# Kernel tuning notes

Measured on AMD Instinct MI355X. Metric: run time of the kernel, lower is better.

Reference implementation:

```python
import jax, jax.numpy as jnp
import numpy as np

D_MODEL = 256
D_STATE = 16
D_INNER = 512          # expand=2 * d_model
D_CONV = 4
DT_RANK = 16           # ceil(d_model/16)
B, L = 16, 2048


def setup_inputs() -> dict:
    key = jax.random.key(0)
    ks = jax.random.split(key, 10)
    s = 0.02
    inp = {
        "x": jax.random.normal(ks[0], (B, L, D_MODEL), dtype=jnp.float32),
        "ln_w": jnp.ones((D_MODEL,), jnp.float32),
        "ln_b": jnp.zeros((D_MODEL,), jnp.float32),
        "in_proj_w": jax.random.normal(ks[1], (2 * D_INNER, D_MODEL)) * s,
        "conv_w": jax.random.normal(ks[2], (D_INNER, 1, D_CONV)) * s,
        "conv_b": jnp.zeros((D_INNER,), jnp.float32),
        "x_proj_w": jax.random.normal(ks[3], (DT_RANK + 2 * D_STATE, D_INNER)) * s,
        "dt_proj_w": jax.random.normal(ks[4], (D_INNER, DT_RANK)) * s,
        "dt_proj_b": jax.random.uniform(ks[5], (D_INNER,), minval=-4.0, maxval=-2.0),
        "A_log": jnp.log(jnp.broadcast_to(jnp.arange(1, D_STATE + 1, dtype=jnp.float32), (D_INNER, D_STATE))).copy(),
        "D_param": jnp.ones((D_INNER,), jnp.float32),
        "out_proj_w": jax.random.normal(ks[6], (D_MODEL, D_INNER)) * s,
    }
    return inp


def _layernorm(x, w, b, eps=1e-5):
    mu = jnp.mean(x, axis=-1, keepdims=True)
    var = jnp.var(x, axis=-1, keepdims=True)
    return (x - mu) * jax.lax.rsqrt(var + eps) * w + b


def _mamba(xn, in_proj_w, conv_w, conv_b, x_proj_w, dt_proj_w, dt_proj_b, A_log, D_param, out_proj_w):
    # in_proj -> x, z   (B, L, d_inner) each
    xz = jnp.einsum('bld,ed->ble', xn, in_proj_w)
    x_in, z = jnp.split(xz, 2, axis=-1)

    # depthwise causal conv over L
    xc = jax.lax.conv_general_dilated(
        jnp.transpose(x_in, (0, 2, 1)), conv_w,
        window_strides=(1,), padding=[(D_CONV - 1, 0)],
        feature_group_count=D_INNER,
        dimension_numbers=('NCH', 'OIH', 'NCH')) + conv_b[None, :, None]
    xc = jax.nn.silu(jnp.transpose(xc, (0, 2, 1)))  # (B, L, d_inner)

    # input-dependent dt, B, C
    dbc = jnp.einsum('ble,fe->blf', xc, x_proj_w)  # (B, L, dt_rank + 2N)
    dt = jax.nn.softplus(jnp.einsum('blr,er->ble', dbc[..., :DT_RANK], dt_proj_w) + dt_proj_b)
    Bc = dbc[..., DT_RANK:DT_RANK + D_STATE]   # (B, L, N)
    Cc = dbc[..., DT_RANK + D_STATE:]          # (B, L, N)

    A = -jnp.exp(A_log)  # (d_inner, N)

    def step(h, inputs):
        dt_t, x_t, B_t, C_t = inputs  # (B,e), (B,e), (B,n), (B,n)
        dA = jnp.exp(dt_t[..., None] * A)                      # (B, e, n)
        h = dA * h + dt_t[..., None] * B_t[:, None, :] * x_t[..., None]
        y = jnp.sum(h * C_t[:, None, :], axis=-1)              # (B, e)
        return h, y

    h0 = jnp.zeros((xn.shape[0], D_INNER, D_STATE), xn.dtype)
    seq = (jnp.swapaxes(dt, 0, 1), jnp.swapaxes(xc, 0, 1),
           jnp.swapaxes(Bc, 0, 1), jnp.swapaxes(Cc, 0, 1))
    _, ys = jax.lax.scan(step, h0, seq)
    y = jnp.swapaxes(ys, 0, 1) + D_param * xc                  # (B, L, e)
    y = y * jax.nn.silu(z)
    return jnp.einsum('ble,de->bld', y, out_proj_w)


def reference(x, ln_w, ln_b, in_proj_w, conv_w, conv_b, x_proj_w, dt_proj_w, dt_proj_b, A_log, D_param, out_proj_w):
    xn = _layernorm(x, ln_w, ln_b)
    out = _mamba(xn, in_proj_w, conv_w, conv_b, x_proj_w, dt_proj_w, dt_proj_b, A_log, D_param, out_proj_w)
    return x + out  # dropout is identity in eval
```

## Files before the change

kernel.cpp:

```cpp
#include <hip/hip_runtime.h>
#include <cstdint>

#define DEVI __device__ __forceinline__

typedef __bf16 bf16;
typedef __bf16 bf16x8 __attribute__((ext_vector_type(8)));
typedef __bf16 bf16x4 __attribute__((ext_vector_type(4)));
typedef __bf16 bf16x2 __attribute__((ext_vector_type(2)));
typedef float floatx4 __attribute__((ext_vector_type(4)));
typedef float f32x2 __attribute__((ext_vector_type(2)));

constexpr int BATCH = 16, SEQ = 2048, DM = 256, DI = 512;
constexpr int M = BATCH * SEQ;
constexpr int NC = 64;
constexpr int CL = SEQ / NC;
static_assert(NC * CL == SEQ, "chunking");
constexpr float LOG2E = 1.4426950408889634f;

DEVI void gl2lds16(const void* g, void* l) {
  __builtin_amdgcn_global_load_lds(
      (const __attribute__((address_space(1))) unsigned int*)(uintptr_t)g,
      (__attribute__((address_space(3))) unsigned int*)(unsigned int)(uintptr_t)l,
      16, 0, 0);
}

DEVI float sigmoidf_(float x) { return 1.f / (1.f + __expf(-x)); }
DEVI float exp2_(float x) { return __builtin_amdgcn_exp2f(x); }

DEVI float bflo(unsigned u) { return __uint_as_float(u << 16); }
DEVI float bfhi(unsigned u) { return __uint_as_float(u & 0xFFFF0000u); }
DEVI f32x2 sp2(float v) { f32x2 r; r[0] = v; r[1] = v; return r; }

DEVI void powseq(f32x2 d, f32x2* P) {
  P[0] = d;
  P[1] = d * d;
  P[2] = P[1] * d;
  P[3] = P[1] * P[1];
  P[4] = P[3] * d;
  P[5] = P[3] * P[1];
  P[6] = P[3] * P[2];
  P[7] = P[3] * P[3];
  P[8] = P[7] * d;
  P[9] = P[7] * P[1];
  P[10] = P[7] * P[2];
  P[11] = P[7] * P[3];
  P[12] = P[7] * P[4];
  P[13] = P[7] * P[5];
  P[14] = P[7] * P[6];
  P[15] = P[7] * P[7];
}

__global__ __launch_bounds__(256) void prep_kernel(
    const float* __restrict__ w1, const float* __restrict__ wx,
    const float* __restrict__ wo, const float* __restrict__ alog,
    bf16* __restrict__ w1b, bf16* __restrict__ wxb, bf16* __restrict__ wob,
    float* __restrict__ An, int* __restrict__ flags) {
  constexpr int n1 = 1024 * 256, n2 = 48 * 512, n3 = 256 * 512;
  int i = blockIdx.x * 256 + threadIdx.x;
  if (i < n1) w1b[i] = (bf16)w1[i];
  else if (i < n1 + n2) wxb[i - n1] = (bf16)wx[i - n1];
  else if (i < n1 + n2 + n3) wob[i - n1 - n2] = (bf16)wo[i - n1 - n2];
  else if (i < n1 + n2 + n3 + DI) {
    const int e = i - (n1 + n2 + n3);
    const float a0 = -__expf(alog[e * 16]);
    bool ok = (a0 < 0.f);
#pragma unroll 1
    for (int s = 0; s < 16; s++) {
      const float a = -__expf(alog[e * 16 + s]);
      An[e * 16 + s] = a * LOG2E;
      ok = ok && (__builtin_fabsf(a / a0 - (float)(s + 1)) < 1e-3f);
    }
    flags[e] = ok ? 1 : 0;
  }
}

__global__ __launch_bounds__(256) void ln_kernel(
    const float* __restrict__ x, const float* __restrict__ w,
    const float* __restrict__ b, bf16* __restrict__ xn) {
  const int row = blockIdx.x * 4 + (threadIdx.x >> 6);
  const int lane = threadIdx.x & 63;
  const float4 v = ((const float4*)(x + (size_t)row * DM))[lane];
  float s = v.x + v.y + v.z + v.w;
  float s2 = v.x * v.x + v.y * v.y + v.z * v.z + v.w * v.w;
#pragma unroll
  for (int m = 1; m < 64; m <<= 1) { s += __shfl_xor(s, m); s2 += __shfl_xor(s2, m); }
  const float mu = s * (1.f / DM);
  const float var = s2 * (1.f / DM) - mu * mu;
  const float rs = rsqrtf(var + 1e-5f);
  const float4 wv = ((const float4*)w)[lane];
  const float4 bv = ((const float4*)b)[lane];
  bf16x4 o;
  o[0] = (bf16)((v.x - mu) * rs * wv.x + bv.x);
  o[1] = (bf16)((v.y - mu) * rs * wv.y + bv.y);
  o[2] = (bf16)((v.z - mu) * rs * wv.z + bv.z);
  o[3] = (bf16)((v.w - mu) * rs * wv.w + bv.w);
  *(bf16x4*)(xn + (size_t)row * DM + lane * 4) = o;
}

template <int N, int K, bool OUT_BF16, bool RESID>
__global__ __launch_bounds__(256) void gemm_nt(const bf16* __restrict__ A,
                                               const bf16* __restrict__ W,
                                               void* __restrict__ out,
                                               const float* __restrict__ resid) {
  constexpr int BK = 32;
  __shared__ __align__(16) bf16 lA[128 * BK];
  __shared__ __align__(16) bf16 lB[128 * BK];
  const int tid = threadIdx.x;
  const int wave = tid >> 6, lane = tid & 63;
  const int bm = blockIdx.x * 128, bn = blockIdx.y * 128;
  const int wm = (wave >> 1) * 64, wn = (wave & 1) * 64;
  const int q = lane >> 4, r = lane & 15;
  floatx4 acc[4][4] = {};
  const int c0 = wave * 64 + lane;
  const int row0 = c0 >> 2, kp = (c0 & 3) * 8;
  for (int k0 = 0; k0 < K; k0 += BK) {
    gl2lds16(A + (size_t)(bm + row0) * K + k0 + kp, lA + c0 * 8);
    gl2lds16(A + (size_t)(bm + row0 + 64) * K + k0 + kp, lA + (c0 + 256) * 8);
    gl2lds16(W + (size_t)(bn + row0) * K + k0 + kp, lB + c0 * 8);
    gl2lds16(W + (size_t)(bn + row0 + 64) * K + k0 + kp, lB + (c0 + 256) * 8);
    __syncthreads();
    bf16x8 af[4], bfr[4];
#pragma unroll
    for (int i = 0; i < 4; i++) af[i] = *(const bf16x8*)&lA[(wm + i * 16 + r) * BK + q * 8];
#pragma unroll
    for (int j = 0; j < 4; j++) bfr[j] = *(const bf16x8*)&lB[(wn + j * 16 + r) * BK + q * 8];
#pragma unroll
    for (int i = 0; i < 4; i++)
#pragma unroll
      for (int j = 0; j < 4; j++)
        acc[i][j] = __builtin_amdgcn_mfma_f32_16x16x32_bf16(af[i], bfr[j], acc[i][j], 0, 0, 0);
    __syncthreads();
  }
#pragma unroll
  for (int i = 0; i < 4; i++)
#pragma unroll
    for (int j = 0; j < 4; j++)
#pragma unroll
      for (int t = 0; t < 4; t++) {
        const int row = bm + wm + i * 16 + q * 4 + t;
        const int col = bn + wn + j * 16 + r;
        const size_t idx = (size_t)row * N + col;
        float v = acc[i][j][t];
        if constexpr (OUT_BF16) {
          ((bf16*)out)[idx] = (bf16)v;
        } else {
          if constexpr (RESID) v += resid[idx];
          ((float*)out)[idx] = v;
        }
      }
}

__global__ __launch_bounds__(256) void conv_silu(const bf16* __restrict__ xz,
                                                 const float* __restrict__ cw,
                                                 const float* __restrict__ cb,
                                                 bf16* __restrict__ xc) {
  const int tid = threadIdx.x;
  const int e2 = tid * 2;
  const int p0 = blockIdx.x * 8;
  const int b = blockIdx.y;
  const float4 w0 = ((const float4*)cw)[e2];
  const float4 w1 = ((const float4*)cw)[e2 + 1];
  const float2 bias = *(const float2*)(cb + e2);
  float xa[11], xb_[11];
#pragma unroll
  for (int j = 0; j < 11; j++) {
    const int pos = p0 - 3 + j;
    float fa = 0.f, fb = 0.f;
    if (pos >= 0) {
      const unsigned u = *(const unsigned*)(xz + ((size_t)b * SEQ + pos) * 1024 + e2);
      fa = __uint_as_float(u << 16);
      fb = __uint_as_float(u & 0xFFFF0000u);
    }
    xa[j] = fa; xb_[j] = fb;
  }
#pragma unroll
  for (int k = 0; k < 8; k++) {
    const float a0 = bias.x + xa[k] * w0.x + xa[k + 1] * w0.y + xa[k + 2] * w0.z + xa[k + 3] * w0.w;
    const float a1 = bias.y + xb_[k] * w1.x + xb_[k + 1] * w1.y + xb_[k + 2] * w1.z + xb_[k + 3] * w1.w;
    bf16x2 o;
    o[0] = (bf16)(a0 * sigmoidf_(a0));
    o[1] = (bf16)(a1 * sigmoidf_(a1));
    *(bf16x2*)(xc + ((size_t)b * SEQ + p0 + k) * DI + e2) = o;
  }
}

__global__ __launch_bounds__(256) void gemm_xproj(const bf16* __restrict__ A,
                                                  const bf16* __restrict__ W,
                                                  float* __restrict__ out) {
  constexpr int K = DI;
  __shared__ __align__(16) bf16 lW[48 * K];
  __shared__ __align__(16) bf16 lA[64 * 32];
  const int tid = threadIdx.x;
  const int wave = tid >> 6, lane = tid & 63;
  const int bm = blockIdx.x * 64;
  const int q = lane >> 4, r = lane & 15;
#pragma unroll
  for (int rd = 0; rd < 12; rd++) {
    const int c = rd * 256 + tid;
    gl2lds16((const char*)W + (size_t)c * 16, (char*)lW + (size_t)c * 16);
  }
  const int row0 = tid >> 2, kp = (tid & 3) * 8;
  const int wm = wave * 16;
  floatx4 acc[3] = {};
  for (int k0 = 0; k0 < K; k0 += 32) {
    gl2lds16(A + (size_t)(bm + row0) * K + k0 + kp, lA + tid * 8);
    __syncthreads();
    bf16x8 af = *(const bf16x8*)&lA[(wm + r) * 32 + q * 8];
#pragma unroll
    for (int j = 0; j < 3; j++) {
      const bf16x8 bfr = *(const bf16x8*)&lW[(j * 16 + r) * K + k0 + q * 8];
      acc[j] = __builtin_amdgcn_mfma_f32_16x16x32_bf16(af, bfr, acc[j], 0, 0, 0);
    }
    __syncthreads();
  }
#pragma unroll
  for (int j = 0; j < 3; j++)
#pragma unroll
    for (int t = 0; t < 4; t++)
      out[(size_t)(bm + wm + q * 4 + t) * 48 + j * 16 + r] = acc[j][t];
}

__global__ __launch_bounds__(256) void dtproj_kernel(const float* __restrict__ dbc,
                                                     const float* __restrict__ dtw,
                                                     const float* __restrict__ dtb,
                                                     bf16* __restrict__ dt) {
  __shared__ __align__(16) float sd[64 * 16];
  const int tid = threadIdx.x;
  const int p0 = blockIdx.x * 64;
  const int e = blockIdx.y * 256 + tid;
  {
    const int rowi = tid >> 2, coli = (tid & 3) * 4;
    *(float4*)&sd[rowi * 16 + coli] = *(const float4*)(dbc + (size_t)(p0 + rowi) * 48 + coli);
  }
  float w[16];
#pragma unroll
  for (int s = 0; s < 16; s += 4) {
    float4 t4 = *(const float4*)(dtw + (size_t)e * 16 + s);
    w[s] = t4.x; w[s + 1] = t4.y; w[s + 2] = t4.z; w[s + 3] = t4.w;
  }
  const float bias = dtb[e];
  __syncthreads();
  for (int p = 0; p < 64; p++) {
    float s = bias;
#pragma unroll
    for (int r2 = 0; r2 < 16; r2++) s += sd[p * 16 + r2] * w[r2];
    const float sp = (s > 15.f) ? s : __logf(1.f + __expf(s));
    dt[(size_t)(p0 + p) * DI + e] = (bf16)sp;
  }
}

__global__ __launch_bounds__(256) void scan_pass1(const bf16* __restrict__ dt,
                                                  const bf16* __restrict__ xc,
                                                  const float* __restrict__ dbc,
                                                  const float* __restrict__ An,
                                                  const int* __restrict__ flags,
                                                  float* __restrict__ U,
                                                  float* __restrict__ SD) {
  __shared__ __align__(16) float sbc[CL * 16];
  const int tid = threadIdx.x;
  const int e2 = tid * 2;
  const int ch = blockIdx.x, b = blockIdx.y;
  const size_t posBase = (size_t)b * SEQ + (size_t)ch * CL;
  if (tid < CL * 4) {
    const int il = tid >> 2, f = (tid & 3) * 4;
    gl2lds16(dbc + (posBase + il) * 48 + 16 + f, (char*)sbc + tid * 16);
  }
  const int2 fl = *(const int2*)(flags + e2);
  const int fast = fl.x & fl.y;
  f32x2 h[16];
#pragma unroll
  for (int s = 0; s < 16; s++) { h[s][0] = 0.f; h[s][1] = 0.f; }
  f32x2 sdt2; sdt2[0] = 0.f; sdt2[1] = 0.f;
  f32x2 A02; A02[0] = An[(size_t)e2 * 16]; A02[1] = An[(size_t)e2 * 16 + 16];
  float Aa[16], Ab[16];
  if (!fast) {
#pragma unroll
    for (int s = 0; s < 16; s += 4) {
      float4 a4 = *(const float4*)(An + (size_t)e2 * 16 + s);
      Aa[s] = a4.x; Aa[s + 1] = a4.y; Aa[s + 2] = a4.z; Aa[s + 3] = a4.w;
      float4 b4 = *(const float4*)(An + (size_t)e2 * 16 + 16 + s);
      Ab[s] = b4.x; Ab[s + 1] = b4.y; Ab[s + 2] = b4.z; Ab[s + 3] = b4.w;
    }
  }
  const char* pdt = (const char*)(dt + posBase * DI + e2);
  const char* pxc = (const char*)(xc + posBase * DI + e2);
  unsigned ud = *(const unsigned*)pdt;
  unsigned ux = *(const unsigned*)pxc;
  __syncthreads();
  if (fast) {
#pragma unroll 1
    for (int il = 0; il < CL; il++) {
      const int np = (il + 1 < CL) ? (il + 1) : il;
      const unsigned nud = *(const unsigned*)(pdt + (size_t)np * DI * 2);
      const unsigned nux = *(const unsigned*)(pxc + (size_t)np * DI * 2);
      f32x2 dt2; dt2[0] = bflo(ud); dt2[1] = bfhi(ud);
      f32x2 xv2; xv2[0] = bflo(ux); xv2[1] = bfhi(ux);
      const f32x2 dtx2 = dt2 * xv2;
      sdt2 = sdt2 + dt2;
      const f32x2 t = dt2 * A02;
      f32x2 d; d[0] = exp2_(t[0]); d[1] = exp2_(t[1]);
      f32x2 P[16];
      powseq(d, P);
      const float4* bb = (const float4*)(sbc + il * 16);
#pragma unroll
      for (int g = 0; g < 4; g++) {
        const float4 B4 = bb[g];
        h[4 * g + 0] = P[4 * g + 0] * h[4 * g + 0] + dtx2 * sp2(B4.x);
        h[4 * g + 1] = P[4 * g + 1] * h[4 * g + 1] + dtx2 * sp2(B4.y);
        h[4 * g + 2] = P[4 * g + 2] * h[4 * g + 2] + dtx2 * sp2(B4.z);
        h[4 * g + 3] = P[4 * g + 3] * h[4 * g + 3] + dtx2 * sp2(B4.w);
      }
      ud = nud; ux = nux;
    }
  } else {
#pragma unroll 1
    for (int il = 0; il < CL; il++) {
      const int np = (il + 1 < CL) ? (il + 1) : il;
      const unsigned nud = *(const unsigned*)(pdt + (size_t)np * DI * 2);
      const unsigned nux = *(const unsigned*)(pxc + (size_t)np * DI * 2);
      const float dta = bflo(ud), dtb_v = bfhi(ud);
      const float xa = bflo(ux), xb = bfhi(ux);
      const float dtxa = dta * xa, dtxb = dtb_v * xb;
      sdt2[0] += dta; sdt2[1] += dtb_v;
      const float* bc = sbc + il * 16;
#pragma unroll
      for (int s = 0; s < 16; s++) {
        const float bv = bc[s];
        h[s][0] = exp2_(dta * Aa[s]) * h[s][0] + dtxa * bv;
        h[s][1] = exp2_(dtb_v * Ab[s]) * h[s][1] + dtxb * bv;
      }
      ud = nud; ux = nux;
    }
  }
  float* up = U + ((size_t)(b * NC + ch) * DI + e2) * 16;
#pragma unroll
  for (int i = 0; i < 4; i++) {
    float4 o; o.x = h[4 * i][0]; o.y = h[4 * i + 1][0]; o.z = h[4 * i + 2][0]; o.w = h[4 * i + 3][0];
    ((float4*)up)[i] = o;
  }
#pragma unroll
  for (int i = 0; i < 4; i++) {
    float4 o; o.x = h[4 * i][1]; o.y = h[4 * i + 1][1]; o.z = h[4 * i + 2][1]; o.w = h[4 * i + 3][1];
    ((float4*)up)[4 + i] = o;
  }
  float2 sdo; sdo.x = sdt2[0]; sdo.y = sdt2[1];
  *(float2*)(SD + (size_t)(b * NC + ch) * DI + e2) = sdo;
}

__global__ __launch_bounds__(256) void scan_pass2(const float* __restrict__ SD,
                                                  float* U,
                                                  const float* __restrict__ An) {
  const int t = blockIdx.x * 256 + threadIdx.x;
  const int s = t & 15;
  const int e = (t >> 4) & (DI - 1);
  const int b = t >> 13;
  const float A = An[e * 16 + s];
  float h = 0.f;
#pragma unroll 4
  for (int c = 0; c < NC; c++) {
    const size_t cell = (size_t)(b * NC + c) * DI + e;
    const float sdv = SD[cell];
    const size_t base = cell * 16 + s;
    const float u = U[base];
    const float h0 = h;
    h = exp2_(A * sdv) * h0 + u;
    U[base] = h0;
  }
}

__global__ __launch_bounds__(256) void scan_pass3(const bf16* __restrict__ dt,
                                                  const bf16* __restrict__ xc,
                                                  const bf16* __restrict__ xz,
                                                  const float* __restrict__ dbc,
                                                  const float* __restrict__ An,
                                                  const int* __restrict__ flags,
                                                  const float* __restrict__ H0,
                                                  const float* __restrict__ Dp,
                                                  bf16* __restrict__ yg) {
  __shared__ __align__(16) float sbc[CL * 32];
  const int tid = threadIdx.x;
  const int e2 = tid * 2;
  const int ch = blockIdx.x, b = blockIdx.y;
  const size_t posBase = (size_t)b * SEQ + (size_t)ch * CL;
  {
    const int il = tid >> 3, f = (tid & 7) * 4;
    gl2lds16(dbc + (posBase + il) * 48 + 16 + f, (char*)sbc + tid * 16);
  }
  const int2 fl = *(const int2*)(flags + e2);
  const int fast = fl.x & fl.y;
  f32x2 h[16];
  const float* hp = H0 + ((size_t)(b * NC + ch) * DI + e2) * 16;
#pragma unroll
  for (int i = 0; i < 4; i++) {
    const float4 h4 = ((const float4*)hp)[i];
    h[4 * i][0] = h4.x; h[4 * i + 1][0] = h4.y; h[4 * i + 2][0] = h4.z; h[4 * i + 3][0] = h4.w;
  }
#pragma unroll
  for (int i = 0; i < 4; i++) {
    const float4 h4 = ((const float4*)hp)[4 + i];
    h[4 * i][1] = h4.x; h[4 * i + 1][1] = h4.y; h[4 * i + 2][1] = h4.z; h[4 * i + 3][1] = h4.w;
  }
  const float2 Dv = *(const float2*)(Dp + e2);
  f32x2 Dv2; Dv2[0] = Dv.x; Dv2[1] = Dv.y;
  f32x2 A02; A02[0] = An[(size_t)e2 * 16]; A02[1] = An[(size_t)e2 * 16 + 16];
  float Aa[16], Ab[16];
  if (!fast) {
#pragma unroll
    for (int s = 0; s < 16; s += 4) {
      float4 a4 = *(const float4*)(An + (size_t)e2 * 16 + s);
      Aa[s] = a4.x; Aa[s + 1] = a4.y; Aa[s + 2] = a4.z; Aa[s + 3] = a4.w;
      float4 b4 = *(const float4*)(An + (size_t)e2 * 16 + 16 + s);
      Ab[s] = b4.x; Ab[s + 1] = b4.y; Ab[s + 2] = b4.z; Ab[s + 3] = b4.w;
    }
  }
  const char* pdt = (const char*)(dt + posBase * DI + e2);
  const char* pxc = (const char*)(xc + posBase * DI + e2);
  const char* pxz = (const char*)(xz + posBase * 1024 + DI + e2);
  unsigned ud = *(const unsigned*)pdt;
  unsigned ux = *(const unsigned*)pxc;
  unsigned uz = *(const unsigned*)pxz;
  __syncthreads();
  if (fast) {
#pragma unroll 1
    for (int il = 0; il < CL; il++) {
      const int np = (il + 1 < CL) ? (il + 1) : il;
      const unsigned nud = *(const unsigned*)(pdt + (size_t)np * DI * 2);
      const unsigned nux = *(const unsigned*)(pxc + (size_t)np * DI * 2);
      const unsigned nuz = *(const unsigned*)(pxz + (size_t)np * 1024 * 2);
      const size_t pos = posBase + il;
      f32x2 dt2; dt2[0] = bflo(ud); dt2[1] = bfhi(ud);
      f32x2 xv2; xv2[0] = bflo(ux); xv2[1] = bfhi(ux);
      f32x2 z2; z2[0] = bflo(uz); z2[1] = bfhi(uz);
      const f32x2 dtx2 = dt2 * xv2;
      const f32x2 t = dt2 * A02;
      f32x2 d; d[0] = exp2_(t[0]); d[1] = exp2_(t[1]);
      f32x2 P[16];
      powseq(d, P);
      const float4* bb = (const float4*)(sbc + il * 32);
      f32x2 Yv[4];
#pragma unroll
      for (int g = 0; g < 4; g++) { Yv[g][0] = 0.f; Yv[g][1] = 0.f; }
#pragma unroll
      for (int g = 0; g < 4; g++) {
        const float4 B4 = bb[g];
        const float4 C4 = bb[4 + g];
        h[4 * g + 0] = P[4 * g + 0] * h[4 * g + 0] + dtx2 * sp2(B4.x);
        Yv[g] = Yv[g] + h[4 * g + 0] * sp2(C4.x);
        h[4 * g + 1] = P[4 * g + 1] * h[4 * g + 1] + dtx2 * sp2(B4.y);
        Yv[g] = Yv[g] + h[4 * g + 1] * sp2(C4.y);
        h[4 * g + 2] = P[4 * g + 2] * h[4 * g + 2] + dtx2 * sp2(B4.z);
        Yv[g] = Yv[g] + h[4 * g + 2] * sp2(C4.z);
        h[4 * g + 3] = P[4 * g + 3] * h[4 * g + 3] + dtx2 * sp2(B4.w);
        Yv[g] = Yv[g] + h[4 * g + 3] * sp2(C4.w);
      }
      const f32x2 Ys = (Yv[0] + Yv[1]) + (Yv[2] + Yv[3]);
      f32x2 gz; gz[0] = z2[0] * sigmoidf_(z2[0]); gz[1] = z2[1] * sigmoidf_(z2[1]);
      const f32x2 yv2 = (Ys + Dv2 * xv2) * gz;
      bf16x2 o; o[0] = (bf16)yv2[0]; o[1] = (bf16)yv2[1];
      *(bf16x2*)(yg + pos * DI + e2) = o;
      ud = nud; ux = nux; uz = nuz;
    }
  } else {
#pragma unroll 1
    for (int il = 0; il < CL; il++) {
      const int np = (il + 1 < CL) ? (il + 1) : il;
      const unsigned nud = *(const unsigned*)(pdt + (size_t)np * DI * 2);
      const unsigned nux = *(const unsigned*)(pxc + (size_t)np * DI * 2);
      const unsigned nuz = *(const unsigned*)(pxz + (size_t)np * 1024 * 2);
      const size_t pos = posBase + il;
      const float dta = bflo(ud), dtb_v = bfhi(ud);
      const float xa = bflo(ux), xb = bfhi(ux);
      const float za = bflo(uz), zb = bfhi(uz);
      const float dtxa = dta * xa, dtxb = dtb_v * xb;
      const float* bc = sbc + il * 32;
      float ya = 0.f, yb = 0.f;
#pragma unroll
      for (int s = 0; s < 16; s++) {
        const float bv = bc[s], cv = bc[16 + s];
        const float ha = exp2_(dta * Aa[s]) * h[s][0] + dtxa * bv;
        const float hb = exp2_(dtb_v * Ab[s]) * h[s][1] + dtxb * bv;
        h[s][0] = ha; h[s][1] = hb;
        ya += ha * cv; yb += hb * cv;
      }
      const float yva = (ya + Dv.x * xa) * za * sigmoidf_(za);
      const float yvb = (yb + Dv.y * xb) * zb * sigmoidf_(zb);
      bf16x2 o; o[0] = (bf16)yva; o[1] = (bf16)yvb;
      *(bf16x2*)(yg + pos * DI + e2) = o;
      ud = nud; ux = nux; uz = nuz;
    }
  }
}

extern "C" void kernel_launch(void* const* d_in, const int* in_sizes, int n_in,
                              void* d_out, int out_size, void* d_ws, size_t ws_size,
                              hipStream_t stream) {
  const float* x = (const float*)d_in[0];
  const float* ln_w = (const float*)d_in[1];
  const float* ln_b = (const float*)d_in[2];
  const float* w_in = (const float*)d_in[3];
  const float* conv_w = (const float*)d_in[4];
  const float* conv_b = (const float*)d_in[5];
  const float* w_x = (const float*)d_in[6];
  const float* w_dt = (const float*)d_in[7];
  const float* b_dt = (const float*)d_in[8];
  const float* a_log = (const float*)d_in[9];
  const float* d_par = (const float*)d_in[10];
  const float* w_out = (const float*)d_in[11];

  char* ws = (char*)d_ws;
  size_t off = 0;
  auto alloc = [&](size_t bytes) {
    void* p = ws + off;
    off = (off + bytes + 255) & ~(size_t)255;
    return p;
  };
  bf16* xn = (bf16*)alloc((size_t)M * DM * 2);
  bf16* xzb = (bf16*)alloc((size_t)M * 1024 * 2);
  bf16* xcb = (bf16*)alloc((size_t)M * DI * 2);
  float* dbc = (float*)alloc((size_t)M * 48 * 4);
  bf16* dtb_ = (bf16*)alloc((size_t)M * DI * 2);
  bf16* ygb = (bf16*)alloc((size_t)M * DI * 2);
  float* U = (float*)alloc((size_t)BATCH * NC * DI * 16 * 4);
  float* SD = (float*)alloc((size_t)BATCH * NC * DI * 4);
  bf16* w1b = (bf16*)alloc(1024 * 256 * 2);
  bf16* wxb = (bf16*)alloc(48 * 512 * 2);
  bf16* wob = (bf16*)alloc(256 * 512 * 2);
  float* An = (float*)alloc(512 * 16 * 4);
  int* flags = (int*)alloc(512 * 4);

  constexpr int prep_n = 1024 * 256 + 48 * 512 + 256 * 512 + DI;
  prep_kernel<<<dim3((prep_n + 255) / 256), dim3(256), 0, stream>>>(w_in, w_x, w_out, a_log, w1b, wxb, wob, An, flags);
  ln_kernel<<<dim3(M / 4), dim3(256), 0, stream>>>(x, ln_w, ln_b, xn);
  gemm_nt<1024, 256, true, false><<<dim3(M / 128, 8), dim3(256), 0, stream>>>(xn, w1b, (void*)xzb, nullptr);
  conv_silu<<<dim3(SEQ / 8, BATCH), dim3(256), 0, stream>>>(xzb, conv_w, conv_b, xcb);
  gemm_xproj<<<dim3(M / 64), dim3(256), 0, stream>>>(xcb, wxb, dbc);
  dtproj_kernel<<<dim3(M / 64, 2), dim3(256), 0, stream>>>(dbc, w_dt, b_dt, dtb_);
  scan_pass1<<<dim3(NC, BATCH), dim3(256), 0, stream>>>(dtb_, xcb, dbc, An, flags, U, SD);
  scan_pass2<<<dim3(BATCH * DI * 16 / 256), dim3(256), 0, stream>>>(SD, U, An);
  scan_pass3<<<dim3(NC, BATCH), dim3(256), 0, stream>>>(dtb_, xcb, xzb, dbc, An, flags, U, d_par, ygb);
  gemm_nt<256, 512, false, true><<<dim3(M / 128, 2), dim3(256), 0, stream>>>(ygb, wob, d_out, x);
}
```

Baseline: 306.7 us.

## Remap GEMM tiles per XCD and software-pipeline chunk-state scan loads

The GEMM grid becomes 1D, and block ids are remapped so that each of the 8 XCDs handles a contiguous range of M tiles with all N tiles of a row. This is meant to improve L2 reuse of A rows within an XCD. Separately, scan_pass2 now double-buffers its serial chain over chunks: it prefetches 16 chunks of SD and U into registers while computing on the previous 16. This hides global-load latency in the dependent recurrence, at the cost of higher register use.

Result: no change. 301.3 us (-1.8%).

```diff
diff --git a/kernel.cpp b/kernel.cpp
--- a/kernel.cpp
+++ b/kernel.cpp
@@ -103,11 +103,17 @@
                                                void* __restrict__ out,
                                                const float* __restrict__ resid) {
   constexpr int BK = 32;
+  constexpr int NB = N / 128;
+  constexpr int MT_PER = (M / 128) / 8;
   __shared__ __align__(16) bf16 lA[128 * BK];
   __shared__ __align__(16) bf16 lB[128 * BK];
   const int tid = threadIdx.x;
+  const int id = blockIdx.x;
+  const int xcd = id & 7;
+  const int local = id >> 3;
+  const int bm = (xcd * MT_PER + local / NB) * 128;
+  const int bn = (local % NB) * 128;
   const int wave = tid >> 6, lane = tid & 63;
-  const int bm = blockIdx.x * 128, bn = blockIdx.y * 128;
   const int wm = (wave >> 1) * 64, wn = (wave & 1) * 64;
   const int q = lane >> 4, r = lane & 15;
   floatx4 acc[4][4] = {};
@@ -354,17 +360,41 @@
   const int s = t & 15;
   const int e = (t >> 4) & (DI - 1);
   const int b = t >> 13;
-  const float A = An[e * 16 + s];
+  const float Av = An[e * 16 + s];
+  const float* sdp = SD + (size_t)b * NC * DI + e;
+  float* up = U + ((size_t)b * NC * DI + e) * 16 + s;
+  float sA_[16], uA_[16], sB_[16], uB_[16];
+#pragma unroll
+  for (int j = 0; j < 16; j++) {
+    sA_[j] = sdp[(size_t)j * DI];
+    uA_[j] = up[(size_t)j * DI * 16];
+  }
   float h = 0.f;
-#pragma unroll 4
-  for (int c = 0; c < NC; c++) {
-    const size_t cell = (size_t)(b * NC + c) * DI + e;
-    const float sdv = SD[cell];
-    const size_t base = cell * 16 + s;
-    const float u = U[base];
-    const float h0 = h;
-    h = exp2_(A * sdv) * h0 + u;
-    U[base] = h0;
+#pragma unroll 1
+  for (int c0 = 0; c0 < NC; c0 += 32) {
+#pragma unroll
+    for (int j = 0; j < 16; j++) {
+      sB_[j] = sdp[(size_t)(c0 + 16 + j) * DI];
+      uB_[j] = up[(size_t)(c0 + 16 + j) * DI * 16];
+    }
+#pragma unroll
+    for (int j = 0; j < 16; j++) {
+      const float h0 = h;
+      h = exp2_(Av * sA_[j]) * h0 + uA_[j];
+      up[(size_t)(c0 + j) * DI * 16] = h0;
+    }
+    const int nn = (c0 + 32 < NC) ? (c0 + 32) : (NC - 16);
+#pragma unroll
+    for (int j = 0; j < 16; j++) {
+      sA_[j] = sdp[(size_t)(nn + j) * DI];
+      uA_[j] = up[(size_t)(nn + j) * DI * 16];
+    }
+#pragma unroll
+    for (int j = 0; j < 16; j++) {
+      const float h0 = h;
+      h = exp2_(Av * sB_[j]) * h0 + uB_[j];
+      up[(size_t)(c0 + 16 + j) * DI * 16] = h0;
+    }
   }
 }
 
@@ -531,12 +561,12 @@
   constexpr int prep_n = 1024 * 256 + 48 * 512 + 256 * 512 + DI;
   prep_kernel<<<dim3((prep_n + 255) / 256), dim3(256), 0, stream>>>(w_in, w_x, w_out, a_log, w1b, wxb, wob, An, flags);
   ln_kernel<<<dim3(M / 4), dim3(256), 0, stream>>>(x, ln_w, ln_b, xn);
-  gemm_nt<1024, 256, true, false><<<dim3(M / 128, 8), dim3(256), 0, stream>>>(xn, w1b, (void*)xzb, nullptr);
+  gemm_nt<1024, 256, true, false><<<dim3((M / 128) * 8), dim3(256), 0, stream>>>(xn, w1b, (void*)xzb, nullptr);
   conv_silu<<<dim3(SEQ / 8, BATCH), dim3(256), 0, stream>>>(xzb, conv_w, conv_b, xcb);
   gemm_xproj<<<dim3(M / 64), dim3(256), 0, stream>>>(xcb, wxb, dbc);
   dtproj_kernel<<<dim3(M / 64, 2), dim3(256), 0, stream>>>(dbc, w_dt, b_dt, dtb_);
   scan_pass1<<<dim3(NC, BATCH), dim3(256), 0, stream>>>(dtb_, xcb, dbc, An, flags, U, SD);
   scan_pass2<<<dim3(BATCH * DI * 16 / 256), dim3(256), 0, stream>>>(SD, U, An);
   scan_pass3<<<dim3(NC, BATCH), dim3(256), 0, stream>>>(dtb_, xcb, xzb, dbc, An, flags, U, d_par, ygb);
-  gemm_nt<256, 512, false, true><<<dim3(M / 128, 2), dim3(256), 0, stream>>>(ygb, wob, d_out, x);
-}
+  gemm_nt<256, 512, false, true><<<dim3((M / 128) * 2), dim3(256), 0, stream>>>(ygb, wob, d_out, x);
+}
```
